# Kernel optimization log

Hardware: AMD Instinct MI355X
Metric: run time of the kernel (lower is better)

## Reference

```python
import jax, jax.numpy as jnp
import numpy as np

B, S, H, D_MODEL, D_HEAD = 2, 2048, 12, 768, 64
INIT_RANGE = 0.02
IGNORE = -100000.0


def setup_inputs() -> dict:
    key = jax.random.key(0)
    ks = jax.random.split(key, 11)
    return {
        "normalized_resid_pre_q": jax.random.normal(ks[0], (B, S, H, D_MODEL), jnp.float32),
        "normalized_resid_pre_k": jax.random.normal(ks[1], (B, S, H, D_MODEL), jnp.float32),
        "normalized_resid_pre_v": jax.random.normal(ks[2], (B, S, H, D_MODEL), jnp.float32),
        "W_Q": jax.random.normal(ks[3], (H, D_MODEL, D_HEAD), jnp.float32) * INIT_RANGE,
        "b_Q": jnp.zeros((H, D_HEAD), jnp.float32),
        "W_K": jax.random.normal(ks[4], (H, D_MODEL, D_HEAD), jnp.float32) * INIT_RANGE,
        "b_K": jnp.zeros((H, D_HEAD), jnp.float32),
        "W_V": jax.random.normal(ks[5], (H, D_MODEL, D_HEAD), jnp.float32) * INIT_RANGE,
        "b_V": jnp.zeros((H, D_HEAD), jnp.float32),
        "W_O": jax.random.normal(ks[6], (H, D_HEAD, D_MODEL), jnp.float32) * INIT_RANGE,
        "b_O": jnp.zeros((D_MODEL,), jnp.float32),
    }


def reference(normalized_resid_pre_q, normalized_resid_pre_k, normalized_resid_pre_v,
              W_Q, b_Q, W_K, b_K, W_V, b_V, W_O, b_O):
    n_heads = W_Q.shape[0]
    d_head = W_Q.shape[-1]
    # per-head projections: input already carries a head axis
    q = jnp.einsum("bqhm,hmd->bqhd", normalized_resid_pre_q, W_Q) + b_Q
    k = jnp.einsum("bkhm,hmd->bkhd", normalized_resid_pre_k, W_K) + b_K
    v = jnp.einsum("bkhm,hmd->bkhd", normalized_resid_pre_v, W_V) + b_V
    scores = jnp.einsum("bqhd,bkhd->bhqk", q, k) / jnp.sqrt(jnp.float32(d_head))
    S_q, S_k = scores.shape[-2], scores.shape[-1]
    causal = jnp.triu(jnp.ones((S_q, S_k), bool), k=1)
    scores = jnp.where(causal, jnp.float32(IGNORE), scores)
    pattern = jax.nn.softmax(scores, axis=-1)
    z = jnp.einsum("bhqk,bkhd->bqhd", pattern, v)
    # output keeps the per-head axis; bias split evenly across heads
    attn_out = jnp.einsum("bqhd,hdm->bqhm", z, W_O) + b_O / n_heads
    return attn_out
```

## Files before the change

kernel.cpp:

```cpp
#include <hip/hip_runtime.h>
#include <hip/hip_bf16.h>
#include <stdint.h>

#define H 12
#define S 2048
#define BATCH 2
#define DM 768
#define DH 64

typedef __attribute__((ext_vector_type(4))) float f32x4;
typedef __attribute__((ext_vector_type(4))) short s16x4;
typedef __attribute__((ext_vector_type(8))) short s16x8;

static __device__ __forceinline__ short f2bf(float f) {
  uint32_t u = __builtin_bit_cast(uint32_t, f);
  uint32_t r = (u + 0x7FFFu + ((u >> 16) & 1u)) >> 16;
  return (short)r;
}

static __device__ __forceinline__ s16x8 cvt8(f32x4 a, f32x4 b) {
  s16x8 r;
  r[0] = f2bf(a[0]); r[1] = f2bf(a[1]); r[2] = f2bf(a[2]); r[3] = f2bf(a[3]);
  r[4] = f2bf(b[0]); r[5] = f2bf(b[1]); r[6] = f2bf(b[2]); r[7] = f2bf(b[3]);
  return r;
}

static __device__ __forceinline__ f32x4 zero4() {
  f32x4 v; v[0] = 0.f; v[1] = 0.f; v[2] = 0.f; v[3] = 0.f; return v;
}

#define GLD_LDS16(g, l)                                                              \
  __builtin_amdgcn_global_load_lds((__attribute__((address_space(1))) const void*)(g), \
                                   (__attribute__((address_space(3))) void*)(l), 16, 0, 0)

#define WAITV(N) asm volatile("s_waitcnt vmcnt(" #N ")" ::: "memory")
#define WAITL0() asm volatile("s_waitcnt lgkmcnt(0)" ::: "memory")
#define BAR() __builtin_amdgcn_s_barrier()
#define FENCE() asm volatile("" ::: "memory")

__global__ __launch_bounds__(256) void k_prep(const float* __restrict__ wq,
                                              const float* __restrict__ wk,
                                              const float* __restrict__ wv,
                                              const float* __restrict__ wo,
                                              short* __restrict__ wt,
                                              short* __restrict__ wot) {
  int tid = blockIdx.x * 256 + threadIdx.x;
  int nthr = gridDim.x * 256;
  const int NQKV = 3 * H * DM * DH;
  for (int i = tid; i < NQKV; i += nthr) {
    int n = i & 63;
    int k = (i >> 6) % DM;
    int rest = (i >> 6) / DM;
    int h = rest % H;
    int t = rest / H;
    const float* src = (t == 0 ? wq : t == 1 ? wk : wv);
    float v = src[((size_t)h * DM + k) * DH + n];
    wt[(((size_t)t * H + h) * DH + n) * DM + k] = f2bf(v);
  }
  const int NO = H * DH * DM;
  for (int i = tid; i < NO; i += nthr) {
    int m = i % DM;
    int d = (i / DM) % DH;
    int h = i / (DM * DH);
    wot[((size_t)h * DM + m) * DH + d] = f2bf(wo[((size_t)h * DH + d) * DM + m]);
  }
}

__global__ __launch_bounds__(256) void k_proj(
    const float* __restrict__ xq, const float* __restrict__ xk, const float* __restrict__ xv,
    const float* __restrict__ bq, const float* __restrict__ bk, const float* __restrict__ bv,
    const short* __restrict__ wt,
    short* __restrict__ q_ws, short* __restrict__ k_ws, short* __restrict__ vt_ws) {
  const int u = blockIdx.x;
  const int xcd = u & 7;
  const int slot = u >> 3;
  const int r = (slot / 12) * 8 + xcd;
  const int h = slot % 12;
  const int t = r / 64;
  const int rb = r % 64;
  const int b = rb >> 5;
  const int q0 = (rb & 31) * 64;

  const float* x = (t == 0 ? xq : t == 1 ? xk : xv);
  const float* xbase = x + ((size_t)(b * S + q0) * H + h) * DM;
  const short* wbase = wt + ((size_t)t * H + h) * (size_t)DH * DM;

  __shared__ float A_sm[2][64 * 64];
  __shared__ short W_sm[2][64 * 64];

  const int tid = threadIdx.x;
  const int w = tid >> 6;
  const int l = tid & 63;
  const int g = l >> 4;
  const int m16 = l & 15;
  const int wswz = ((l & 7) ^ (l >> 3)) * 8;

  const int arow_st = (l >> 4);
  const int apb = (l & 15) * 16;

  f32x4 acc[4];
#pragma unroll
  for (int nt = 0; nt < 4; ++nt) acc[nt] = zero4();

#define PROJ_STAGE(sel, kc)                                                          \
  do {                                                                               \
    _Pragma("unroll") for (int i = 0; i < 4; ++i) {                                  \
      int row = (w * 4 + i) * 4 + arow_st;                                           \
      int colf = (apb ^ ((row & 7) << 4)) >> 2;                                      \
      GLD_LDS16(xbase + (size_t)row * (H * DM) + (kc) * 64 + colf,                   \
                (char*)A_sm + (sel) * 16384 + (w * 4 + i) * 1024);                   \
    }                                                                                \
    _Pragma("unroll") for (int i = 0; i < 2; ++i) {                                  \
      int ch = w * 2 + i;                                                            \
      int n = ch * 8 + (l >> 3);                                                     \
      GLD_LDS16(wbase + (size_t)n * DM + (kc) * 64 + wswz,                           \
                (char*)W_sm + (sel) * 8192 + ch * 1024);                             \
    }                                                                                \
  } while (0)

#define PROJ_COMPUTE(sel)                                                            \
  do {                                                                               \
    const char* Ab = (const char*)A_sm + (sel) * 16384;                              \
    const char* Wb = (const char*)W_sm + (sel) * 8192;                               \
    int arow = 16 * w + m16;                                                         \
    int asw = (arow & 7) << 4;                                                       \
    _Pragma("unroll") for (int c = 0; c < 2; ++c) {                                  \
      f32x4 a0 = *(const f32x4*)(Ab + arow * 256 + ((32 * g + 128 * c) ^ asw));      \
      f32x4 a1 = *(const f32x4*)(Ab + arow * 256 + ((32 * g + 128 * c + 16) ^ asw)); \
      s16x8 afr = cvt8(a0, a1);                                                      \
      int krow = 8 * g + 32 * c;                                                     \
      _Pragma("unroll") for (int nt = 0; nt < 4; ++nt) {                             \
        int n = m16 + 16 * nt;                                                       \
        s16x8 bfr = *(const s16x8*)(Wb + ((n * 128 + krow * 2) ^ ((n & 7) << 4)));   \
        acc[nt] = __builtin_amdgcn_mfma_f32_16x16x32_bf16(afr, bfr, acc[nt], 0, 0, 0); \
      }                                                                              \
    }                                                                                \
  } while (0)

  PROJ_STAGE(0, 0);
#pragma unroll
  for (int kc = 0; kc < 12; ++kc) {
    const int cur = kc & 1;
    if (kc < 11) {
      PROJ_STAGE(cur ^ 1, kc + 1);
      WAITV(6);
    } else {
      WAITV(0);
    }
    BAR(); FENCE();
    PROJ_COMPUTE(cur);
    WAITL0(); BAR(); FENCE();
  }

  const float* bias = (t == 0 ? bq : t == 1 ? bk : bv) + h * DH;
  if (t < 2) {
    short* dst = (t == 0 ? q_ws : k_ws) + (size_t)(b * H + h) * S * DH;
#pragma unroll
    for (int nt = 0; nt < 4; ++nt) {
      int n = 16 * nt + m16;
      float bb = bias[n];
#pragma unroll
      for (int r2 = 0; r2 < 4; ++r2) {
        int q = q0 + 16 * w + 4 * g + r2;
        dst[(size_t)q * DH + n] = f2bf(acc[nt][r2] + bb);
      }
    }
  } else {
    short* dst = vt_ws + (size_t)(b * H + h) * DH * S;
#pragma unroll
    for (int nt = 0; nt < 4; ++nt) {
      int n = 16 * nt + m16;
      float bb = bias[n];
#pragma unroll
      for (int r2 = 0; r2 < 4; ++r2) {
        int q = q0 + 16 * w + 4 * g + r2;
        dst[(size_t)n * S + q] = f2bf(acc[nt][r2] + bb);
      }
    }
  }
}

__global__ __launch_bounds__(256) void k_attn_o(const short* __restrict__ q_ws,
                                                const short* __restrict__ k_ws,
                                                const short* __restrict__ vt_ws,
                                                const short* __restrict__ wot,
                                                const float* __restrict__ bo,
                                                float* __restrict__ out) {
  const int u = blockIdx.x;
  const int xcd = u & 7;
  const int slot = u >> 3;
  const int r = (slot / 12) * 8 + xcd;
  const int h = slot % 12;
  const int b = r >> 5;
  const int qtile = 31 - (r & 31);
  const int q0 = qtile * 64;

  const size_t sl = (size_t)(b * H + h) * S * DH;
  const short* qs = q_ws + sl;
  const short* ks = k_ws + sl;
  const short* vs = vt_ws + sl;

  __shared__ short K_sm[2][64 * 64];
  __shared__ short V_sm[2][64 * 64];
  __shared__ short P_sm[4][16 * 72];

  const int tid = threadIdx.x;
  const int w = tid >> 6;
  const int l = tid & 63;
  const int g = l >> 4;
  const int m16 = l & 15;
  const int swz_src = ((l & 7) ^ (l >> 3)) * 8;

#define ATTN_STAGE(sel, kv0)                                                         \
  do {                                                                               \
    _Pragma("unroll") for (int i = 0; i < 2; ++i) {                                  \
      int ch = w * 2 + i;                                                            \
      int row = ch * 8 + (l >> 3);                                                   \
      GLD_LDS16(ks + (size_t)((kv0) + row) * DH + swz_src,                           \
                (char*)K_sm + (sel) * 8192 + ch * 1024);                             \
      GLD_LDS16(vs + (size_t)row * S + (kv0) + swz_src,                              \
                (char*)V_sm + (sel) * 8192 + ch * 1024);                             \
    }                                                                                \
  } while (0)

  s16x8 qf[2];
  {
    int q = q0 + 16 * w + m16;
    qf[0] = *(const s16x8*)(qs + (size_t)q * DH + 8 * g);
    qf[1] = *(const s16x8*)(qs + (size_t)q * DH + 8 * g + 32);
  }

  f32x4 o_acc[4];
  float m_run[4], l_run[4], alpha[4];
#pragma unroll
  for (int nt = 0; nt < 4; ++nt) o_acc[nt] = zero4();
#pragma unroll
  for (int rr = 0; rr < 4; ++rr) { m_run[rr] = -3.0e38f; l_run[rr] = 0.f; }

  const int ktiles = qtile + 1;
  ATTN_STAGE(0, 0);
  for (int kt = 0; kt < ktiles; ++kt) {
    const int kv0 = kt * 64;
    const int cur = kt & 1;
    if (kt + 1 < ktiles) {
      ATTN_STAGE(cur ^ 1, kv0 + 64);
      WAITV(4);
    } else {
      WAITV(0);
    }
    BAR(); FENCE();

    f32x4 sacc[4];
#pragma unroll
    for (int nt = 0; nt < 4; ++nt) sacc[nt] = zero4();
#pragma unroll
    for (int c = 0; c < 2; ++c) {
      int kr2 = (8 * g + 32 * c) * 2;
#pragma unroll
      for (int nt = 0; nt < 4; ++nt) {
        int row = m16 + 16 * nt;
        s16x8 kf = *(const s16x8*)((const char*)K_sm + cur * 8192 +
                                   ((row * 128 + kr2) ^ ((row & 7) << 4)));
        sacc[nt] = __builtin_amdgcn_mfma_f32_16x16x32_bf16(qf[c], kf, sacc[nt], 0, 0, 0);
      }
    }
    float sv[4][4];
#pragma unroll
    for (int nt = 0; nt < 4; ++nt) {
      int kv = kv0 + 16 * nt + m16;
#pragma unroll
      for (int rr = 0; rr < 4; ++rr) {
        int q = q0 + 16 * w + 4 * g + rr;
        float s = sacc[nt][rr] * 0.125f;
        sv[nt][rr] = (kv > q) ? -1.0e30f : s;
      }
    }
#pragma unroll
    for (int rr = 0; rr < 4; ++rr) {
      float tm = fmaxf(fmaxf(sv[0][rr], sv[1][rr]), fmaxf(sv[2][rr], sv[3][rr]));
      tm = fmaxf(tm, __shfl_xor(tm, 1));
      tm = fmaxf(tm, __shfl_xor(tm, 2));
      tm = fmaxf(tm, __shfl_xor(tm, 4));
      tm = fmaxf(tm, __shfl_xor(tm, 8));
      float mn = fmaxf(m_run[rr], tm);
      alpha[rr] = __expf(m_run[rr] - mn);
      m_run[rr] = mn;
      float rs = 0.f;
#pragma unroll
      for (int nt = 0; nt < 4; ++nt) {
        float p = __expf(sv[nt][rr] - mn);
        sv[nt][rr] = p;
        rs += p;
      }
      rs += __shfl_xor(rs, 1);
      rs += __shfl_xor(rs, 2);
      rs += __shfl_xor(rs, 4);
      rs += __shfl_xor(rs, 8);
      l_run[rr] = l_run[rr] * alpha[rr] + rs;
    }
#pragma unroll
    for (int nt = 0; nt < 4; ++nt)
#pragma unroll
      for (int rr = 0; rr < 4; ++rr)
        P_sm[w][(4 * g + rr) * 72 + 16 * nt + m16] = f2bf(sv[nt][rr]);
#pragma unroll
    for (int nt = 0; nt < 4; ++nt)
#pragma unroll
      for (int rr = 0; rr < 4; ++rr) o_acc[nt][rr] *= alpha[rr];
#pragma unroll
    for (int c = 0; c < 2; ++c) {
      s16x8 pf = *(const s16x8*)(&P_sm[w][m16 * 72 + 8 * g + 32 * c]);
      int kv2 = (8 * g + 32 * c) * 2;
#pragma unroll
      for (int nt = 0; nt < 4; ++nt) {
        int d = m16 + 16 * nt;
        s16x8 vf = *(const s16x8*)((const char*)V_sm + cur * 8192 +
                                   ((d * 128 + kv2) ^ ((d & 7) << 4)));
        o_acc[nt] = __builtin_amdgcn_mfma_f32_16x16x32_bf16(pf, vf, o_acc[nt], 0, 0, 0);
      }
    }
    WAITL0(); BAR(); FENCE();
  }

  short* Z_sm = (short*)K_sm;
  char* WO_sm = (char*)V_sm;
  float* bo_lds = (float*)P_sm;
  const short* wos = wot + (size_t)h * DM * DH;

#define STAGE_WO(sel, nc)                                                            \
  do {                                                                               \
    _Pragma("unroll") for (int i = 0; i < 2; ++i) {                                  \
      int ch = w * 2 + i;                                                            \
      int row = ch * 8 + (l >> 3);                                                   \
      GLD_LDS16(wos + (size_t)((nc) * 64 + row) * DH + swz_src,                      \
                WO_sm + (sel) * 8192 + ch * 1024);                                   \
    }                                                                                \
  } while (0)

  STAGE_WO(0, 0);
  for (int i = tid; i < DM; i += 256) bo_lds[i] = bo[i] * (1.0f / 12.0f);
#pragma unroll
  for (int nt = 0; nt < 4; ++nt) {
#pragma unroll
    for (int rr = 0; rr < 4; ++rr) {
      int row = 16 * w + 4 * g + rr;
      int d = 16 * nt + m16;
      int byte = (row * 128 + d * 2) ^ ((row & 7) << 4);
      *(short*)((char*)Z_sm + byte) = f2bf(o_acc[nt][rr] / l_run[rr]);
    }
  }
  WAITL0(); BAR(); FENCE();

  s16x8 af[2];
#pragma unroll
  for (int c = 0; c < 2; ++c) {
    int row = 16 * w + m16;
    int kr2 = (8 * g + 32 * c) * 2;
    af[c] = *(const s16x8*)((const char*)Z_sm + ((row * 128 + kr2) ^ ((row & 7) << 4)));
  }

#pragma unroll
  for (int nc = 0; nc < 12; ++nc) {
    const int cur = nc & 1;
    if (nc < 11) {
      STAGE_WO(cur ^ 1, nc + 1);
      if (nc == 0) { WAITV(2); }
      else        { WAITV(18); }
    } else {
      WAITV(0);
    }
    BAR(); FENCE();
    f32x4 acc[4];
#pragma unroll
    for (int nt = 0; nt < 4; ++nt) acc[nt] = zero4();
#pragma unroll
    for (int c = 0; c < 2; ++c) {
      int kr2 = (8 * g + 32 * c) * 2;
#pragma unroll
      for (int nt = 0; nt < 4; ++nt) {
        int row = m16 + 16 * nt;
        s16x8 bf = *(const s16x8*)(WO_sm + cur * 8192 +
                                   ((row * 128 + kr2) ^ ((row & 7) << 4)));
        acc[nt] = __builtin_amdgcn_mfma_f32_16x16x32_bf16(af[c], bf, acc[nt], 0, 0, 0);
      }
    }
#pragma unroll
    for (int nt = 0; nt < 4; ++nt) {
      int m = nc * 64 + 16 * nt + m16;
      float bias = bo_lds[m];
#pragma unroll
      for (int rr = 0; rr < 4; ++rr) {
        int q = q0 + 16 * w + 4 * g + rr;
        out[((size_t)(b * S + q) * H + h) * DM + m] = acc[nt][rr] + bias;
      }
    }
    WAITL0(); BAR(); FENCE();
  }
#undef STAGE_WO
#undef ATTN_STAGE
}

extern "C" void kernel_launch(void* const* d_in, const int* in_sizes, int n_in,
                              void* d_out, int out_size, void* d_ws, size_t ws_size,
                              hipStream_t stream) {
  const float* xq = (const float*)d_in[0];
  const float* xk = (const float*)d_in[1];
  const float* xv = (const float*)d_in[2];
  const float* wq = (const float*)d_in[3];
  const float* bq = (const float*)d_in[4];
  const float* wk = (const float*)d_in[5];
  const float* bk = (const float*)d_in[6];
  const float* wv = (const float*)d_in[7];
  const float* bv = (const float*)d_in[8];
  const float* wo = (const float*)d_in[9];
  const float* bo = (const float*)d_in[10];
  float* out = (float*)d_out;

  short* wt = (short*)d_ws;
  short* wot = wt + (size_t)3 * H * DH * DM;
  short* q_ws = wot + (size_t)H * DM * DH;
  short* k_ws = q_ws + (size_t)BATCH * H * S * DH;
  short* vt_ws = k_ws + (size_t)BATCH * H * S * DH;

  k_prep<<<dim3(1024), dim3(256), 0, stream>>>(wq, wk, wv, wo, wt, wot);
  k_proj<<<dim3(2304), dim3(256), 0, stream>>>(xq, xk, xv, bq, bk, bv, wt, q_ws, k_ws, vt_ws);
  k_attn_o<<<dim3(768), dim3(256), 0, stream>>>(q_ws, k_ws, vt_ws, wot, bo, out);
}
```

Before: 219.0 us.

## Triple-buffer projection loads and stage output-projection tiles through LDS for vectorized stores

The projection kernel moves from double to triple buffering, prefetching two K-chunks ahead with adjusted vmcnt waits to hide more global load latency. The attention kernel's output projection now writes each 64x64 fp32 tile into a swizzled LDS buffer, then reads it back so each thread stores 16-byte vectors to global memory, replacing scattered scalar stores. This adds LDS usage, which may lower occupancy, and an extra barrier per output chunk.

```diff
diff --git a/kernel.cpp b/kernel.cpp
--- a/kernel.cpp
+++ b/kernel.cpp
@@ -85,8 +85,8 @@
   const float* xbase = x + ((size_t)(b * S + q0) * H + h) * DM;
   const short* wbase = wt + ((size_t)t * H + h) * (size_t)DH * DM;
 
-  __shared__ float A_sm[2][64 * 64];
-  __shared__ short W_sm[2][64 * 64];
+  __shared__ float A_sm[3][64 * 64];
+  __shared__ short W_sm[3][64 * 64];
 
   const int tid = threadIdx.x;
   const int w = tid >> 6;
@@ -138,17 +138,20 @@
   } while (0)
 
   PROJ_STAGE(0, 0);
+  PROJ_STAGE(1, 1);
 #pragma unroll
   for (int kc = 0; kc < 12; ++kc) {
-    const int cur = kc & 1;
-    if (kc < 11) {
-      PROJ_STAGE(cur ^ 1, kc + 1);
+    const int sel = kc % 3;
+    if (kc < 10) {
+      PROJ_STAGE((kc + 2) % 3, kc + 2);
+      WAITV(12);
+    } else if (kc == 10) {
       WAITV(6);
     } else {
       WAITV(0);
     }
     BAR(); FENCE();
-    PROJ_COMPUTE(cur);
+    PROJ_COMPUTE(sel);
     WAITL0(); BAR(); FENCE();
   }
 
@@ -325,6 +328,7 @@
   short* Z_sm = (short*)K_sm;
   char* WO_sm = (char*)V_sm;
   float* bo_lds = (float*)P_sm;
+  float* obuf = (float*)K_sm;
   const short* wos = wot + (size_t)h * DM * DH;
 
 #define STAGE_WO(sel, nc)                                                            \
@@ -358,6 +362,7 @@
     int kr2 = (8 * g + 32 * c) * 2;
     af[c] = *(const s16x8*)((const char*)Z_sm + ((row * 128 + kr2) ^ ((row & 7) << 4)));
   }
+  WAITL0(); BAR(); FENCE();
 
 #pragma unroll
   for (int nc = 0; nc < 12; ++nc) {
@@ -365,14 +370,14 @@
     if (nc < 11) {
       STAGE_WO(cur ^ 1, nc + 1);
       if (nc == 0) { WAITV(2); }
-      else        { WAITV(18); }
+      else        { WAITV(6); }
     } else {
-      WAITV(0);
+      WAITV(4);
     }
     BAR(); FENCE();
-    f32x4 acc[4];
-#pragma unroll
-    for (int nt = 0; nt < 4; ++nt) acc[nt] = zero4();
+    f32x4 acc2[4];
+#pragma unroll
+    for (int nt = 0; nt < 4; ++nt) acc2[nt] = zero4();
 #pragma unroll
     for (int c = 0; c < 2; ++c) {
       int kr2 = (8 * g + 32 * c) * 2;
@@ -381,18 +386,28 @@
         int row = m16 + 16 * nt;
         s16x8 bf = *(const s16x8*)(WO_sm + cur * 8192 +
                                    ((row * 128 + kr2) ^ ((row & 7) << 4)));
-        acc[nt] = __builtin_amdgcn_mfma_f32_16x16x32_bf16(af[c], bf, acc[nt], 0, 0, 0);
+        acc2[nt] = __builtin_amdgcn_mfma_f32_16x16x32_bf16(af[c], bf, acc2[nt], 0, 0, 0);
       }
     }
 #pragma unroll
     for (int nt = 0; nt < 4; ++nt) {
-      int m = nc * 64 + 16 * nt + m16;
-      float bias = bo_lds[m];
 #pragma unroll
       for (int rr = 0; rr < 4; ++rr) {
-        int q = q0 + 16 * w + 4 * g + rr;
-        out[((size_t)(b * S + q) * H + h) * DM + m] = acc[nt][rr] + bias;
-      }
+        int ql = 16 * w + 4 * g + rr;
+        int ml = 16 * nt + m16;
+        int sw = ((ql >> 2) & 3) << 4;
+        obuf[ql * 64 + (ml ^ sw)] = acc2[nt][rr] + bo_lds[nc * 64 + ml];
+      }
+    }
+    WAITL0(); BAR(); FENCE();
+#pragma unroll
+    for (int s = 0; s < 4; ++s) {
+      int idx = tid + 256 * s;
+      int row = idx >> 4;
+      int ms = idx & 15;
+      int sw = ((row >> 2) & 3) << 4;
+      f32x4 v = *(const f32x4*)(obuf + row * 64 + ((ms * 4) ^ sw));
+      *(f32x4*)(out + ((size_t)(b * S + q0 + row) * H + h) * DM + nc * 64 + ms * 4) = v;
     }
     WAITL0(); BAR(); FENCE();
   }
```

Result: slower. 225.0 us (+2.8%).
